# Optimization experiments

Measured on AMD Instinct MI355X. Metric: run time of the kernel, lower is better.

The kernel has to match this reference:

```python
import jax, jax.numpy as jnp
import numpy as np

B, H, W, C, N, P = 4, 200, 176, 256, 16384, 65536
EPS = 1e-3  # BatchNorm eps from the torch module


def _bn(x, g, b, axes):
    # training-mode batch norm (batch statistics), matching nn.BatchNorm forward
    m = x.mean(axes, keepdims=True)
    v = x.var(axes, keepdims=True)
    return (x - m) * jax.lax.rsqrt(v + EPS) * g + b


def setup_inputs() -> dict:
    key = jax.random.key(0)
    ks = jax.random.split(key, 16)
    s = 0.05
    d = {}
    d['feats'] = jax.random.normal(ks[0], (B, C, N), jnp.float32)
    d['cb'] = jax.random.randint(ks[1], (P,), 0, B, dtype=jnp.int32)
    d['cy'] = jax.random.randint(ks[2], (P,), 0, H, dtype=jnp.int32)
    d['cx'] = jax.random.randint(ks[3], (P,), 0, W, dtype=jnp.int32)
    # SH head: Linear(256,256,nb)+BN+ReLU, Linear(256,256,nb)+BN+ReLU, Linear(256,9,b)
    d['sh_w1'] = jax.random.normal(ks[4], (C, 256), jnp.float32) * s
    d['sh_g1'] = jnp.ones((256,), jnp.float32); d['sh_b1'] = jnp.zeros((256,), jnp.float32)
    d['sh_w2'] = jax.random.normal(ks[5], (256, 256), jnp.float32) * s
    d['sh_g2'] = jnp.ones((256,), jnp.float32); d['sh_b2'] = jnp.zeros((256,), jnp.float32)
    d['sh_w3'] = jax.random.normal(ks[6], (256, 9), jnp.float32) * s
    d['sh_bias3'] = jnp.zeros((9,), jnp.float32)
    # Gaus head: Linear(256,256,nb)+BN+ReLU, Linear(256,128,nb)+BN+ReLU, Linear(128,1,b)+sigmoid
    d['g_w1'] = jax.random.normal(ks[7], (C, 256), jnp.float32) * s
    d['g_g1'] = jnp.ones((256,), jnp.float32); d['g_b1'] = jnp.zeros((256,), jnp.float32)
    d['g_w2'] = jax.random.normal(ks[8], (256, 128), jnp.float32) * s
    d['g_g2'] = jnp.ones((128,), jnp.float32); d['g_b2'] = jnp.zeros((128,), jnp.float32)
    d['g_w3'] = jax.random.normal(ks[9], (128, 1), jnp.float32) * s
    d['g_bias3'] = jnp.zeros((1,), jnp.float32)
    # conv_out: 3x3 SparseConv2d no-bias + BN + ReLU ; shared_conv: 3x3 SubMConv2d bias + BN + ReLU
    d['cw1'] = jax.random.normal(ks[10], (3, 3, C, C), jnp.float32) * s
    d['c1_g'] = jnp.ones((C,), jnp.float32); d['c1_b'] = jnp.zeros((C,), jnp.float32)
    d['cw2'] = jax.random.normal(ks[11], (3, 3, C, C), jnp.float32) * s
    d['c2_bias'] = jnp.zeros((C,), jnp.float32)
    d['c2_g'] = jnp.ones((C,), jnp.float32); d['c2_b'] = jnp.zeros((C,), jnp.float32)
    return d


def reference(feats, cb, cy, cx, sh_w1, sh_g1, sh_b1, sh_w2, sh_g2, sh_b2, sh_w3, sh_bias3,
              g_w1, g_g1, g_b1, g_w2, g_g2, g_b2, g_w3, g_bias3,
              cw1, c1_g, c1_b, cw2, c2_bias, c2_g, c2_b):
    # [B,C,N] -> [B*N, C] point-wise features
    pw = feats.transpose(0, 2, 1).reshape(-1, C)
    # pool_feature_in_same_voxel: mean of point features sharing a voxel
    vid = cb * (H * W) + cy * W + cx  # [P] linear voxel id over dense BEV grid
    S = B * H * W
    sums = jax.ops.segment_sum(pw, vid, num_segments=S)            # [S, C]
    cnt = jax.ops.segment_sum(jnp.ones((P,), pw.dtype), vid, num_segments=S)
    pooled = sums / jnp.maximum(cnt, 1.0)[:, None]                 # [S, C]
    # SH head
    h = jax.nn.relu(_bn(pooled @ sh_w1, sh_g1, sh_b1, 0))
    h = jax.nn.relu(_bn(h @ sh_w2, sh_g2, sh_b2, 0))
    pred_sh = h @ sh_w3 + sh_bias3                                 # [S, 9]
    # Gaussian head
    g = jax.nn.relu(_bn(pooled @ g_w1, g_g1, g_b1, 0))
    g = jax.nn.relu(_bn(g @ g_w2, g_g2, g_b2, 0))
    pred_gaus = jax.nn.sigmoid(g @ g_w3 + g_bias3)                 # [S, 1]
    # get_sparse_voxel_feature3: SH (DC term) + gaussian modulated voxel features
    sp = pooled * pred_gaus * pred_sh[:, :1]                       # [S, C]
    x = sp.reshape(B, H, W, C)                                      # dense BEV sparse-tensor equivalent
    dn = ('NHWC', 'HWIO', 'NHWC')
    x = jax.lax.conv_general_dilated(x, cw1, (1, 1), 'SAME', dimension_numbers=dn)
    x = jax.nn.relu(_bn(x, c1_g, c1_b, (0, 1, 2)))
    x = jax.lax.conv_general_dilated(x, cw2, (1, 1), 'SAME', dimension_numbers=dn) + c2_bias
    x = jax.nn.relu(_bn(x, c2_g, c2_b, (0, 1, 2)))
    return x
```

## Files before the change

### kernel.cpp

```cpp
#include <hip/hip_runtime.h>
#include <hip/hip_bf16.h>
#include <cstdint>
#include <cstddef>

#define B_DIM 4
#define H_DIM 200
#define W_DIM 176
#define CCH 256
#define NPP 16384
#define NPTS 65536
#define HW 35200
#define S_TOT 140800
#define EPS 1e-3f
#define INV_S (1.0f/140800.0f)

typedef unsigned short ushort_t;
typedef __attribute__((ext_vector_type(8))) short bf16x8;
typedef __attribute__((ext_vector_type(4))) float f32x4;

__device__ __forceinline__ ushort_t f2bf(float f) {
    __hip_bfloat16 h = __float2bfloat16(f);
    return *(ushort_t*)&h;
}
__device__ __forceinline__ float bf2f(ushort_t u) {
    __hip_bfloat16 h = *(__hip_bfloat16*)&u;
    return __bfloat162float(h);
}

__device__ __forceinline__ void async16(const void* g, void* l) {
    __builtin_amdgcn_global_load_lds(
        (const __attribute__((address_space(1))) unsigned int*)g,
        (__attribute__((address_space(3))) unsigned int*)l,
        16, 0, 0);
}

__device__ __forceinline__ int xcd_virt(int fid, int n) {
    int q = n >> 3, r = n & 7;
    int xcd = fid & 7, idx = fid >> 3;
    int base = (xcd < r) ? xcd * (q + 1) : r * (q + 1) + (xcd - r) * q;
    return base + idx;
}

__global__ __launch_bounds__(256) void k_transpose(
    const float* __restrict__ feats, float* __restrict__ FT)
{
    __shared__ float lds[64][65];
    const int b  = blockIdx.z;
    const int c0 = blockIdx.y * 64;
    const int n0 = blockIdx.x * 64;
    const int tid = threadIdx.x;
#pragma unroll
    for (int i = 0; i < 16; ++i) {
        int idx = i * 256 + tid;
        int cr = idx >> 6, nc = idx & 63;
        lds[cr][nc] = feats[((size_t)b * 256 + c0 + cr) * NPP + n0 + nc];
    }
    __syncthreads();
#pragma unroll
    for (int i = 0; i < 16; ++i) {
        int idx = i * 256 + tid;
        int nr = idx >> 6, cc = idx & 63;
        FT[((size_t)b * NPP + n0 + nr) * CCH + c0 + cc] = lds[cc][nr];
    }
}

__global__ __launch_bounds__(256) void k_buildidx(
    const int* __restrict__ cb, const int* __restrict__ cy,
    const int* __restrict__ cx, int* __restrict__ cnt,
    int* __restrict__ pslot, int* __restrict__ vid)
{
    int p = blockIdx.x * 256 + threadIdx.x;
    int v = cb[p] * HW + cy[p] * W_DIM + cx[p];
    vid[p] = v;
    int r = atomicAdd(&cnt[v], 1);
    if (r < 8) pslot[v * 8 + r] = p;
}

__global__ __launch_bounds__(256) void k_poolgather(
    const float* __restrict__ FT, const int* __restrict__ cnt,
    const int* __restrict__ pslot, const int* __restrict__ vid,
    ushort_t* __restrict__ Pb)
{
    const int wave = threadIdx.x >> 6;
    const int lane = threadIdx.x & 63;
    const int v = blockIdx.x * 4 + wave;
    const int c = cnt[v];
    float4 a = make_float4(0.f, 0.f, 0.f, 0.f);
    if (c <= 8) {
        for (int k = 0; k < c; ++k) {
            int p = pslot[v * 8 + k];
            float4 r = ((const float4*)(FT + (size_t)p * CCH))[lane];
            a.x += r.x; a.y += r.y; a.z += r.z; a.w += r.w;
        }
    } else {
        for (int p = 0; p < NPTS; ++p)
            if (vid[p] == v) {
                float4 r = ((const float4*)(FT + (size_t)p * CCH))[lane];
                a.x += r.x; a.y += r.y; a.z += r.z; a.w += r.w;
            }
    }
    float inv = c ? 1.f / (float)c : 0.f;
    ushort4 o;
    o.x = f2bf(a.x * inv); o.y = f2bf(a.y * inv);
    o.z = f2bf(a.z * inv); o.w = f2bf(a.w * inv);
    ((ushort4*)(Pb + (size_t)v * CCH))[lane] = o;
}

__global__ __launch_bounds__(256) void k_gemmma(
    const ushort_t* __restrict__ X, const ushort_t* __restrict__ Wt,
    ushort_t* __restrict__ Yb, int N, int nblocks)
{
    __shared__ ushort_t Asm[128 * 64];
    __shared__ ushort_t Bsm[128 * 64];
    const int tid  = threadIdx.x;
    const int w    = tid >> 6;
    const int lane = tid & 63;
    const int virt = xcd_virt(blockIdx.x, nblocks);
    int pi, bn;
    if (N == 256) { pi = virt >> 1; bn = (virt & 1) * 128; }
    else          { pi = virt;      bn = 0; }
    const int bm = pi * 128;
    const int wr = (w >> 1) * 64;
    const int wc = (w & 1) * 64;

    size_t aoff[4]; size_t boff[4];
#pragma unroll
    for (int j = 0; j < 4; ++j) {
        int row  = 32 * j + 8 * w + (lane >> 3);
        int qlog = (lane & 7) ^ (row & 7);
        aoff[j] = (size_t)(bm + row) * 256 + qlog * 8;
        boff[j] = (size_t)(bn + row) * 256 + qlog * 8;
    }

    f32x4 acc[4][4] = {};
    for (int kc = 0; kc < 256; kc += 64) {
#pragma unroll
        for (int j = 0; j < 4; ++j)
            async16(X + aoff[j] + kc, Asm + (j * 32 + w * 8) * 64);
#pragma unroll
        for (int j = 0; j < 4; ++j)
            async16(Wt + boff[j] + kc, Bsm + (j * 32 + w * 8) * 64);
        __syncthreads();
#pragma unroll
        for (int ks = 0; ks < 2; ++ks) {
            const int q = ks * 4 + (lane >> 4);
            bf16x8 af[4], bfr[4];
#pragma unroll
            for (int i = 0; i < 4; ++i) {
                int ra = wr + i * 16 + (lane & 15);
                af[i] = *(const bf16x8*)&Asm[ra * 64 + ((q ^ (ra & 7)) * 8)];
            }
#pragma unroll
            for (int jn = 0; jn < 4; ++jn) {
                int rn = wc + jn * 16 + (lane & 15);
                bfr[jn] = *(const bf16x8*)&Bsm[rn * 64 + ((q ^ (rn & 7)) * 8)];
            }
#pragma unroll
            for (int i = 0; i < 4; ++i)
#pragma unroll
                for (int jn = 0; jn < 4; ++jn)
                    acc[i][jn] = __builtin_amdgcn_mfma_f32_16x16x32_bf16(
                        af[i], bfr[jn], acc[i][jn], 0, 0, 0);
        }
        __syncthreads();
    }
    const int crow0 = bm + wr + (lane >> 4) * 4;
    const int ccol0 = bn + wc + (lane & 15);
#pragma unroll
    for (int i = 0; i < 4; ++i)
#pragma unroll
        for (int jn = 0; jn < 4; ++jn)
#pragma unroll
            for (int r = 0; r < 4; ++r)
                Yb[(size_t)(crow0 + i * 16 + r) * N + ccol0 + jn * 16] =
                    f2bf(acc[i][jn][r]);
}

__global__ __launch_bounds__(256) void k_convmma(
    const ushort_t* __restrict__ X, const ushort_t* __restrict__ Wt,
    float* __restrict__ Yf, ushort_t* __restrict__ Yb,
    const float* __restrict__ bias, const ushort_t* __restrict__ zp)
{
    __shared__ ushort_t Asm[2][192 * 64];
    __shared__ ushort_t Bsm[2][128 * 64];
    const int tid  = threadIdx.x;
    const int w    = tid >> 6;
    const int lane = tid & 63;
    const int virt = xcd_virt(blockIdx.x, 2200);
    const int pi   = virt >> 1;
    const int bn   = (virt & 1) * 128;
    const int b    = pi / 275;
    const int rem  = pi % 275;
    const int th   = rem / 11, tw = rem % 11;
    const int y0   = th * 8 - 1, x0 = tw * 16 - 1;
    const int hb   = (w >> 1) * 4;
    const int wc   = (w & 1) * 64;

    const int qlog = (lane & 7) ^ (lane >> 3);
    const ushort_t* asrc[6];
#pragma unroll
    for (int j = 0; j < 6; ++j) {
        int hr = j * 32 + w * 8 + (lane >> 3);
        int ph = hr / 18, pw = hr % 18;
        int y = y0 + ph, x = x0 + pw;
        bool ok = (hr < 180) && ((unsigned)y < (unsigned)H_DIM) &&
                  ((unsigned)x < (unsigned)W_DIM);
        asrc[j] = ok ? X + ((size_t)b * HW + (size_t)y * W_DIM + x) * 256 + qlog * 8
                     : zp + (lane & 7) * 8;
    }
    const ushort_t* bsrc = Wt + (size_t)(bn + w * 8 + (lane >> 3)) * 256 + qlog * 8;
    const int ldsoff = (w * 8) * 64;

#pragma unroll
    for (int j = 0; j < 6; ++j)
        async16(asrc[j], &Asm[0][(j * 32) * 64 + ldsoff]);
#pragma unroll
    for (int j = 0; j < 4; ++j)
        async16(bsrc + (size_t)j * 8192, &Bsm[0][(j * 32) * 64 + ldsoff]);
    __syncthreads();

    f32x4 acc[4][4] = {};
    for (int kc = 0; kc < 4; ++kc) {
        const ushort_t* acur = Asm[kc & 1];
#pragma unroll
        for (int pos = 0; pos < 9; ++pos) {
            const ushort_t* bcur = Bsm[(kc + pos) & 1];
            ushort_t* bnxt = (ushort_t*)Bsm[(kc + pos + 1) & 1];
            if (pos < 8) {
#pragma unroll
                for (int j = 0; j < 4; ++j)
                    async16(bsrc + (size_t)(pos + 1) * 65536 + kc * 64 + j * 8192,
                            bnxt + (j * 32) * 64 + ldsoff);
            } else if (kc < 3) {
#pragma unroll
                for (int j = 0; j < 4; ++j)
                    async16(bsrc + (size_t)(kc + 1) * 64 + j * 8192,
                            bnxt + (j * 32) * 64 + ldsoff);
#pragma unroll
                for (int j = 0; j < 6; ++j)
                    async16(asrc[j] + (kc + 1) * 64,
                            &Asm[(kc + 1) & 1][(j * 32) * 64 + ldsoff]);
            }
            const int dy = pos / 3 - 1, dx = pos % 3 - 1;
#pragma unroll
            for (int ks = 0; ks < 2; ++ks) {
                const int q = ks * 4 + (lane >> 4);
                bf16x8 af[4], bfr[4];
#pragma unroll
                for (int i = 0; i < 4; ++i) {
                    int ri = (hb + i + 1 + dy) * 18 + 1 + dx + (lane & 15);
                    af[i] = *(const bf16x8*)&acur[ri * 64 + ((q ^ (ri & 7)) * 8)];
                }
#pragma unroll
                for (int jn = 0; jn < 4; ++jn) {
                    int rn = wc + jn * 16 + (lane & 15);
                    bfr[jn] = *(const bf16x8*)&bcur[rn * 64 + ((q ^ (rn & 7)) * 8)];
                }
#pragma unroll
                for (int i = 0; i < 4; ++i)
#pragma unroll
                    for (int jn = 0; jn < 4; ++jn)
                        acc[i][jn] = __builtin_amdgcn_mfma_f32_16x16x32_bf16(
                            af[i], bfr[jn], acc[i][jn], 0, 0, 0);
            }
            __syncthreads();
        }
    }

    const size_t sbase = (size_t)b * HW + (size_t)(th * 8) * W_DIM + tw * 16;
    const int colb = bn + wc + (lane & 15);
    const int wsub = (lane >> 4) * 4;
#pragma unroll
    for (int i = 0; i < 4; ++i) {
        int h = hb + i;
#pragma unroll
        for (int jn = 0; jn < 4; ++jn) {
            int col = colb + jn * 16;
            float bb = bias ? bias[col] : 0.f;
#pragma unroll
            for (int r = 0; r < 4; ++r) {
                size_t s = sbase + (size_t)h * W_DIM + wsub + r;
                float v = acc[i][jn][r] + bb;
                size_t o = s * 256 + col;
                if (Yb) Yb[o] = f2bf(v); else Yf[o] = v;
            }
        }
    }
}

__global__ __launch_bounds__(256) void k_castw(
    const float* __restrict__ Wc, ushort_t* __restrict__ Wt, int CO)
{
    int pc = blockIdx.x;
    int co = pc % CO, pos = pc / CO, ci = threadIdx.x;
    Wt[(size_t)pc * 256 + ci] = f2bf(Wc[((size_t)pos * 256 + ci) * CO + co]);
}

__global__ void k_colstats_bf(const ushort_t* __restrict__ Y,
                              float* __restrict__ acc)
{
    const int ncols = blockDim.x;
    const int col = threadIdx.x;
    const int r0 = blockIdx.x * 256;
    float s = 0.f, q = 0.f;
    const ushort_t* p = Y + (size_t)r0 * ncols + col;
    for (int r = 0; r < 256; ++r, p += ncols) {
        float v = bf2f(*p);
        s += v; q += v * v;
    }
    atomicAdd(&acc[col], s);
    atomicAdd(&acc[ncols + col], q);
}

__global__ void k_colstats(const float* __restrict__ Y, float* __restrict__ acc)
{
    const int ncols = blockDim.x;
    const int col = threadIdx.x;
    const int r0 = blockIdx.x * 256;
    float s = 0.f, q = 0.f;
    const float* p = Y + (size_t)r0 * ncols + col;
    for (int r = 0; r < 256; ++r, p += ncols) {
        float v = *p;
        s += v; q += v * v;
    }
    atomicAdd(&acc[col], s);
    atomicAdd(&acc[ncols + col], q);
}

__global__ void k_bnparams(const float* __restrict__ acc,
                           const float* __restrict__ g,
                           const float* __restrict__ b,
                           float* __restrict__ par, int ncols)
{
    int c = threadIdx.x;
    if (c >= ncols) return;
    float m = acc[c] * INV_S;
    float v = acc[ncols + c] * INV_S - m * m;
    float sc = g[c] * rsqrtf(v + EPS);
    par[c] = sc;
    par[ncols + c] = b[c] - m * sc;
}

__global__ __launch_bounds__(256) void k_bnrelu_bf(
    ushort_t* __restrict__ Y, const float* __restrict__ par)
{
    size_t q = (size_t)blockIdx.x * 256 + threadIdx.x;
    int c = (int)(q & 63) * 4;
    ushort4 u = ((ushort4*)Y)[q];
    u.x = f2bf(fmaxf(0.f, bf2f(u.x) * par[c + 0] + par[256 + c + 0]));
    u.y = f2bf(fmaxf(0.f, bf2f(u.y) * par[c + 1] + par[256 + c + 1]));
    u.z = f2bf(fmaxf(0.f, bf2f(u.z) * par[c + 2] + par[256 + c + 2]));
    u.w = f2bf(fmaxf(0.f, bf2f(u.w) * par[c + 3] + par[256 + c + 3]));
    ((ushort4*)Y)[q] = u;
}

__global__ __launch_bounds__(256) void k_headfin(
    const ushort_t* __restrict__ B2, const ushort_t* __restrict__ B3,
    const float* __restrict__ par1, const float* __restrict__ par3,
    const float* __restrict__ shw3, const float* __restrict__ shb3,
    const float* __restrict__ gw3, const float* __restrict__ gb3,
    const ushort_t* __restrict__ Pb, ushort_t* __restrict__ Xb)
{
    const int wave = threadIdx.x >> 6;
    const int lane = threadIdx.x & 63;
    const int s = blockIdx.x * 4 + wave;
    const ushort_t* b2 = B2 + (size_t)s * 256;
    const ushort_t* b3 = B3 + (size_t)s * 128;
    float d1 = 0.f, d2 = 0.f;
    {
        ushort4 u = ((const ushort4*)b2)[lane];
        int c = lane * 4;
        float v0 = fmaxf(0.f, bf2f(u.x) * par1[c + 0] + par1[256 + c + 0]);
        float v1 = fmaxf(0.f, bf2f(u.y) * par1[c + 1] + par1[256 + c + 1]);
        float v2 = fmaxf(0.f, bf2f(u.z) * par1[c + 2] + par1[256 + c + 2]);
        float v3 = fmaxf(0.f, bf2f(u.w) * par1[c + 3] + par1[256 + c + 3]);
        d1 = v0 * shw3[(c + 0) * 9] + v1 * shw3[(c + 1) * 9]
           + v2 * shw3[(c + 2) * 9] + v3 * shw3[(c + 3) * 9];
    }
    {
        ushort2 u = ((const ushort2*)b3)[lane];
        int c = lane * 2;
        float v0 = fmaxf(0.f, bf2f(u.x) * par3[c + 0] + par3[128 + c + 0]);
        float v1 = fmaxf(0.f, bf2f(u.y) * par3[c + 1] + par3[128 + c + 1]);
        d2 = v0 * gw3[c + 0] + v1 * gw3[c + 1];
    }
#pragma unroll
    for (int off = 32; off > 0; off >>= 1) {
        d1 += __shfl_down(d1, off, 64);
        d2 += __shfl_down(d2, off, 64);
    }
    d1 = __shfl(d1, 0, 64);
    d2 = __shfl(d2, 0, 64);
    float shdc = d1 + shb3[0];
    float gaus = 1.f / (1.f + expf(-(d2 + gb3[0])));
    float factor = shdc * gaus;
    ushort4 pv = ((const ushort4*)(Pb + (size_t)s * 256))[lane];
    ushort4 o;
    o.x = f2bf(bf2f(pv.x) * factor);
    o.y = f2bf(bf2f(pv.y) * factor);
    o.z = f2bf(bf2f(pv.z) * factor);
    o.w = f2bf(bf2f(pv.w) * factor);
    ((ushort4*)(Xb + (size_t)s * 256))[lane] = o;
}

__global__ __launch_bounds__(256) void k_bnrelu_inplace(
    float* __restrict__ Y, const float* __restrict__ par)
{
    size_t q = (size_t)blockIdx.x * 256 + threadIdx.x;
    int c = (int)(q & 63) * 4;
    float4* p = (float4*)Y;
    float4 v = p[q];
    v.x = fmaxf(0.f, v.x * par[c + 0] + par[256 + c + 0]);
    v.y = fmaxf(0.f, v.y * par[c + 1] + par[256 + c + 1]);
    v.z = fmaxf(0.f, v.z * par[c + 2] + par[256 + c + 2]);
    v.w = fmaxf(0.f, v.w * par[c + 3] + par[256 + c + 3]);
    p[q] = v;
}

extern "C" void kernel_launch(void* const* d_in, const int* in_sizes, int n_in,
                              void* d_out, int out_size, void* d_ws, size_t ws_size,
                              hipStream_t stream)
{
    (void)in_sizes; (void)n_in; (void)out_size; (void)ws_size;
    const float* feats   = (const float*)d_in[0];
    const int*   cb      = (const int*)d_in[1];
    const int*   cy      = (const int*)d_in[2];
    const int*   cx      = (const int*)d_in[3];
    const float* sh_w1   = (const float*)d_in[4];
    const float* sh_g1   = (const float*)d_in[5];
    const float* sh_b1   = (const float*)d_in[6];
    const float* sh_w2   = (const float*)d_in[7];
    const float* sh_g2   = (const float*)d_in[8];
    const float* sh_b2   = (const float*)d_in[9];
    const float* sh_w3   = (const float*)d_in[10];
    const float* sh_bias3= (const float*)d_in[11];
    const float* g_w1    = (const float*)d_in[12];
    const float* g_g1    = (const float*)d_in[13];
    const float* g_b1    = (const float*)d_in[14];
    const float* g_w2    = (const float*)d_in[15];
    const float* g_g2    = (const float*)d_in[16];
    const float* g_b2    = (const float*)d_in[17];
    const float* g_w3    = (const float*)d_in[18];
    const float* g_bias3 = (const float*)d_in[19];
    const float* cw1     = (const float*)d_in[20];
    const float* c1_g    = (const float*)d_in[21];
    const float* c1_b    = (const float*)d_in[22];
    const float* cw2     = (const float*)d_in[23];
    const float* c2_bias = (const float*)d_in[24];
    const float* c2_g    = (const float*)d_in[25];
    const float* c2_b    = (const float*)d_in[26];

    float* out = (float*)d_out;
    float* ws  = (float*)d_ws;
    ushort_t* Pb   = (ushort_t*)(ws);
    ushort_t* Bb   = (ushort_t*)(ws + 18022400);
    ushort_t* Cb   = (ushort_t*)(ws + 36044800);
    float*    FT   = (float*)(ws + 36044800);
    ushort_t* Db   = (ushort_t*)(ws + 54067200);
    int*      CNTi = (int*)(ws + 54067200);
    int*      PSL  = CNTi + S_TOT;
    int*      VID  = PSL + S_TOT * 8;
    ushort_t* Eb   = (ushort_t*)(ws + 63078400);
    ushort_t* WT1  = (ushort_t*)(ws + 81100800);
    ushort_t* WT2  = WT1 + 589824;
    ushort_t* WS1  = WT2 + 589824;
    ushort_t* WS2  = WS1 + 65536;
    ushort_t* WG1  = WS2 + 65536;
    ushort_t* WG2  = WG1 + 65536;
    ushort_t* ZP   = WG2 + 32768;
    float*    ACC  = (float*)(ZP + 2048);
    float*    PAR  = ACC + 6 * 512;

    hipMemsetAsync(CNTi, 0, (size_t)S_TOT * 4, stream);
    hipMemsetAsync(ACC, 0, 6 * 512 * 4, stream);
    hipMemsetAsync(ZP, 0, 4096, stream);

    k_castw<<<9 * 256, 256, 0, stream>>>(cw1, WT1, 256);
    k_castw<<<9 * 256, 256, 0, stream>>>(cw2, WT2, 256);
    k_castw<<<256, 256, 0, stream>>>(sh_w1, WS1, 256);
    k_castw<<<256, 256, 0, stream>>>(sh_w2, WS2, 256);
    k_castw<<<256, 256, 0, stream>>>(g_w1, WG1, 256);
    k_castw<<<128, 256, 0, stream>>>(g_w2, WG2, 128);

    k_transpose<<<dim3(256, 4, 4), 256, 0, stream>>>(feats, FT);
    k_buildidx<<<NPTS / 256, 256, 0, stream>>>(cb, cy, cx, CNTi, PSL, VID);
    k_poolgather<<<S_TOT / 4, 256, 0, stream>>>(FT, CNTi, PSL, VID, Pb);

    k_gemmma<<<2200, 256, 0, stream>>>(Pb, WS1, Bb, 256, 2200);
    k_colstats_bf<<<550, 256, 0, stream>>>(Bb, ACC + 0 * 512);
    k_bnparams<<<1, 256, 0, stream>>>(ACC + 0 * 512, sh_g1, sh_b1, PAR + 0 * 512, 256);
    k_bnrelu_bf<<<35200, 256, 0, stream>>>(Bb, PAR + 0 * 512);
    k_gemmma<<<2200, 256, 0, stream>>>(Bb, WS2, Cb, 256, 2200);
    k_colstats_bf<<<550, 256, 0, stream>>>(Cb, ACC + 1 * 512);
    k_bnparams<<<1, 256, 0, stream>>>(ACC + 1 * 512, sh_g2, sh_b2, PAR + 1 * 512, 256);
    k_gemmma<<<2200, 256, 0, stream>>>(Pb, WG1, Bb, 256, 2200);
    k_colstats_bf<<<550, 256, 0, stream>>>(Bb, ACC + 2 * 512);
    k_bnparams<<<1, 256, 0, stream>>>(ACC + 2 * 512, g_g1, g_b1, PAR + 2 * 512, 256);
    k_bnrelu_bf<<<35200, 256, 0, stream>>>(Bb, PAR + 2 * 512);
    k_gemmma<<<1100, 256, 0, stream>>>(Bb, WG2, Db, 128, 1100);
    k_colstats_bf<<<550, 128, 0, stream>>>(Db, ACC + 3 * 512);
    k_bnparams<<<1, 128, 0, stream>>>(ACC + 3 * 512, g_g2, g_b2, PAR + 3 * 512, 128);
    k_headfin<<<S_TOT / 4, 256, 0, stream>>>(Cb, Db, PAR + 1 * 512, PAR + 3 * 512,
                                             sh_w3, sh_bias3, g_w3, g_bias3, Pb, Bb);
    k_convmma<<<2200, 256, 0, stream>>>(Bb, WT1, nullptr, Eb, nullptr, ZP);
    k_colstats_bf<<<550, 256, 0, stream>>>(Eb, ACC + 4 * 512);
    k_bnparams<<<1, 256, 0, stream>>>(ACC + 4 * 512, c1_g, c1_b, PAR + 4 * 512, 256);
    k_bnrelu_bf<<<35200, 256, 0, stream>>>(Eb, PAR + 4 * 512);
    k_convmma<<<2200, 256, 0, stream>>>(Eb, WT2, out, nullptr, c2_bias, ZP);
    k_colstats<<<550, 256, 0, stream>>>(out, ACC + 5 * 512);
    k_bnparams<<<1, 256, 0, stream>>>(ACC + 5 * 512, c2_g, c2_b, PAR + 5 * 512, 256);
    k_bnrelu_inplace<<<35200, 256, 0, stream>>>(out, PAR + 5 * 512);
}
```

Baseline: 879.4 us.

## Fuse BN column statistics into GEMM/conv epilogues and merge first-layer head GEMMs

Column sum and sum-of-squares for batch norm are now reduced in the epilogues of the MFMA GEMM and conv kernels (shuffle plus LDS reduction, then atomics), which removes six separate colstats passes that re-read the activations. The SH and Gaussian first-layer weights are concatenated so a single GEMM with N=512 reads the pooled input once and writes two outputs. The statistics are taken from fp32 accumulators rather than bf16-rounded values, which slightly changes the numerics. The epilogues gain extra atomics and a block sync, and the workspace layout is reshuffled, with Eb now aliasing Pb.

New measurement: 865.3 us. No clear change (-1.6%).

```diff
diff --git a/kernel.cpp b/kernel.cpp
--- a/kernel.cpp
+++ b/kernel.cpp
@@ -108,7 +108,9 @@
 
 __global__ __launch_bounds__(256) void k_gemmma(
     const ushort_t* __restrict__ X, const ushort_t* __restrict__ Wt,
-    ushort_t* __restrict__ Yb, int N, int nblocks)
+    ushort_t* __restrict__ Y1, ushort_t* __restrict__ Y2, int ldY,
+    int bnh, int nblocks,
+    float* __restrict__ acc0, float* __restrict__ acc1, int sqoff)
 {
     __shared__ ushort_t Asm[128 * 64];
     __shared__ ushort_t Bsm[128 * 64];
@@ -116,12 +118,11 @@
     const int w    = tid >> 6;
     const int lane = tid & 63;
     const int virt = xcd_virt(blockIdx.x, nblocks);
-    int pi, bn;
-    if (N == 256) { pi = virt >> 1; bn = (virt & 1) * 128; }
-    else          { pi = virt;      bn = 0; }
-    const int bm = pi * 128;
-    const int wr = (w >> 1) * 64;
-    const int wc = (w & 1) * 64;
+    const int pi   = virt / bnh;
+    const int bn   = (virt % bnh) * 128;
+    const int bm   = pi * 128;
+    const int wr   = (w >> 1) * 64;
+    const int wc   = (w & 1) * 64;
 
     size_t aoff[4]; size_t boff[4];
 #pragma unroll
@@ -164,22 +165,56 @@
         }
         __syncthreads();
     }
+
     const int crow0 = bm + wr + (lane >> 4) * 4;
     const int ccol0 = bn + wc + (lane & 15);
+    float ls[4] = {}, lq[4] = {};
 #pragma unroll
     for (int i = 0; i < 4; ++i)
 #pragma unroll
-        for (int jn = 0; jn < 4; ++jn)
-#pragma unroll
-            for (int r = 0; r < 4; ++r)
-                Yb[(size_t)(crow0 + i * 16 + r) * N + ccol0 + jn * 16] =
-                    f2bf(acc[i][jn][r]);
+        for (int jn = 0; jn < 4; ++jn) {
+            int col = ccol0 + jn * 16;
+#pragma unroll
+            for (int r = 0; r < 4; ++r) {
+                float v = acc[i][jn][r];
+                ls[jn] += v; lq[jn] += v * v;
+                size_t row = (size_t)(crow0 + i * 16 + r);
+                if (col < 256) Y1[row * ldY + col] = f2bf(v);
+                else           Y2[row * ldY + col - 256] = f2bf(v);
+            }
+        }
+#pragma unroll
+    for (int jn = 0; jn < 4; ++jn) {
+        ls[jn] += __shfl_xor(ls[jn], 16, 64); ls[jn] += __shfl_xor(ls[jn], 32, 64);
+        lq[jn] += __shfl_xor(lq[jn], 16, 64); lq[jn] += __shfl_xor(lq[jn], 32, 64);
+    }
+    float* red = (float*)Asm;
+    if (lane < 16) {
+#pragma unroll
+        for (int jn = 0; jn < 4; ++jn) {
+            red[((w * 16 + lane) * 4 + jn) * 2 + 0] = ls[jn];
+            red[((w * 16 + lane) * 4 + jn) * 2 + 1] = lq[jn];
+        }
+    }
+    __syncthreads();
+    if (tid < 256) {
+        int colhalf = tid & 127, isq = tid >> 7;
+        int pair = colhalf >> 6, within = colhalf & 63;
+        int l16 = within & 15, jn = within >> 4;
+        int w0 = pair ? 1 : 0, w1 = pair ? 3 : 2;
+        float s = red[((w0 * 16 + l16) * 4 + jn) * 2 + isq]
+                + red[((w1 * 16 + l16) * 4 + jn) * 2 + isq];
+        int colg = bn + colhalf;
+        float* t = (colg < 256) ? acc0 : acc1;
+        atomicAdd(&t[(colg & 255) + isq * sqoff], s);
+    }
 }
 
 __global__ __launch_bounds__(256) void k_convmma(
     const ushort_t* __restrict__ X, const ushort_t* __restrict__ Wt,
     float* __restrict__ Yf, ushort_t* __restrict__ Yb,
-    const float* __restrict__ bias, const ushort_t* __restrict__ zp)
+    const float* __restrict__ bias, const ushort_t* __restrict__ zp,
+    float* __restrict__ accp)
 {
     __shared__ ushort_t Asm[2][192 * 64];
     __shared__ ushort_t Bsm[2][128 * 64];
@@ -270,6 +305,7 @@
     const size_t sbase = (size_t)b * HW + (size_t)(th * 8) * W_DIM + tw * 16;
     const int colb = bn + wc + (lane & 15);
     const int wsub = (lane >> 4) * 4;
+    float ls[4] = {}, lq[4] = {};
 #pragma unroll
     for (int i = 0; i < 4; ++i) {
         int h = hb + i;
@@ -281,10 +317,34 @@
             for (int r = 0; r < 4; ++r) {
                 size_t s = sbase + (size_t)h * W_DIM + wsub + r;
                 float v = acc[i][jn][r] + bb;
+                ls[jn] += v; lq[jn] += v * v;
                 size_t o = s * 256 + col;
                 if (Yb) Yb[o] = f2bf(v); else Yf[o] = v;
             }
         }
+    }
+#pragma unroll
+    for (int jn = 0; jn < 4; ++jn) {
+        ls[jn] += __shfl_xor(ls[jn], 16, 64); ls[jn] += __shfl_xor(ls[jn], 32, 64);
+        lq[jn] += __shfl_xor(lq[jn], 16, 64); lq[jn] += __shfl_xor(lq[jn], 32, 64);
+    }
+    float* red = (float*)&Asm[0][0];
+    if (lane < 16) {
+#pragma unroll
+        for (int jn = 0; jn < 4; ++jn) {
+            red[((w * 16 + lane) * 4 + jn) * 2 + 0] = ls[jn];
+            red[((w * 16 + lane) * 4 + jn) * 2 + 1] = lq[jn];
+        }
+    }
+    __syncthreads();
+    if (tid < 256) {
+        int colhalf = tid & 127, isq = tid >> 7;
+        int pair = colhalf >> 6, within = colhalf & 63;
+        int l16 = within & 15, jn = within >> 4;
+        int w0 = pair ? 1 : 0, w1 = pair ? 3 : 2;
+        float s = red[((w0 * 16 + l16) * 4 + jn) * 2 + isq]
+                + red[((w1 * 16 + l16) * 4 + jn) * 2 + isq];
+        atomicAdd(&accp[(bn + colhalf) + isq * 256], s);
     }
 }
 
@@ -294,37 +354,6 @@
     int pc = blockIdx.x;
     int co = pc % CO, pos = pc / CO, ci = threadIdx.x;
     Wt[(size_t)pc * 256 + ci] = f2bf(Wc[((size_t)pos * 256 + ci) * CO + co]);
-}
-
-__global__ void k_colstats_bf(const ushort_t* __restrict__ Y,
-                              float* __restrict__ acc)
-{
-    const int ncols = blockDim.x;
-    const int col = threadIdx.x;
-    const int r0 = blockIdx.x * 256;
-    float s = 0.f, q = 0.f;
-    const ushort_t* p = Y + (size_t)r0 * ncols + col;
-    for (int r = 0; r < 256; ++r, p += ncols) {
-        float v = bf2f(*p);
-        s += v; q += v * v;
-    }
-    atomicAdd(&acc[col], s);
-    atomicAdd(&acc[ncols + col], q);
-}
-
-__global__ void k_colstats(const float* __restrict__ Y, float* __restrict__ acc)
-{
-    const int ncols = blockDim.x;
-    const int col = threadIdx.x;
-    const int r0 = blockIdx.x * 256;
-    float s = 0.f, q = 0.f;
-    const float* p = Y + (size_t)r0 * ncols + col;
-    for (int r = 0; r < 256; ++r, p += ncols) {
-        float v = *p;
-        s += v; q += v * v;
-    }
-    atomicAdd(&acc[col], s);
-    atomicAdd(&acc[ncols + col], q);
 }
 
 __global__ void k_bnparams(const float* __restrict__ acc,
@@ -453,21 +482,21 @@
     float* out = (float*)d_out;
     float* ws  = (float*)d_ws;
     ushort_t* Pb   = (ushort_t*)(ws);
-    ushort_t* Bb   = (ushort_t*)(ws + 18022400);
-    ushort_t* Cb   = (ushort_t*)(ws + 36044800);
-    float*    FT   = (float*)(ws + 36044800);
-    ushort_t* Db   = (ushort_t*)(ws + 54067200);
-    int*      CNTi = (int*)(ws + 54067200);
+    ushort_t* Bsh  = (ushort_t*)(ws + 18022400);
+    ushort_t* Bg   = (ushort_t*)(ws + 36044800);
+    ushort_t* Cb   = (ushort_t*)(ws + 54067200);
+    float*    FT   = (float*)(ws + 54067200);
+    ushort_t* Db   = (ushort_t*)(ws + 72089600);
+    int*      CNTi = (int*)(ws + 72089600);
     int*      PSL  = CNTi + S_TOT;
     int*      VID  = PSL + S_TOT * 8;
-    ushort_t* Eb   = (ushort_t*)(ws + 63078400);
-    ushort_t* WT1  = (ushort_t*)(ws + 81100800);
+    ushort_t* Eb   = Pb;
+    ushort_t* WCAT = (ushort_t*)(ws + 81100800);
+    ushort_t* WS2  = WCAT + 131072;
+    ushort_t* WG2  = WS2 + 65536;
+    ushort_t* WT1  = WG2 + 32768;
     ushort_t* WT2  = WT1 + 589824;
-    ushort_t* WS1  = WT2 + 589824;
-    ushort_t* WS2  = WS1 + 65536;
-    ushort_t* WG1  = WS2 + 65536;
-    ushort_t* WG2  = WG1 + 65536;
-    ushort_t* ZP   = WG2 + 32768;
+    ushort_t* ZP   = WT2 + 589824;
     float*    ACC  = (float*)(ZP + 2048);
     float*    PAR  = ACC + 6 * 512;
 
@@ -475,39 +504,37 @@
     hipMemsetAsync(ACC, 0, 6 * 512 * 4, stream);
     hipMemsetAsync(ZP, 0, 4096, stream);
 
+    k_castw<<<256, 256, 0, stream>>>(sh_w1, WCAT, 256);
+    k_castw<<<256, 256, 0, stream>>>(g_w1, WCAT + 65536, 256);
+    k_castw<<<256, 256, 0, stream>>>(sh_w2, WS2, 256);
+    k_castw<<<128, 256, 0, stream>>>(g_w2, WG2, 128);
     k_castw<<<9 * 256, 256, 0, stream>>>(cw1, WT1, 256);
     k_castw<<<9 * 256, 256, 0, stream>>>(cw2, WT2, 256);
-    k_castw<<<256, 256, 0, stream>>>(sh_w1, WS1, 256);
-    k_castw<<<256, 256, 0, stream>>>(sh_w2, WS2, 256);
-    k_castw<<<256, 256, 0, stream>>>(g_w1, WG1, 256);
-    k_castw<<<128, 256, 0, stream>>>(g_w2, WG2, 128);
 
     k_transpose<<<dim3(256, 4, 4), 256, 0, stream>>>(feats, FT);
     k_buildidx<<<NPTS / 256, 256, 0, stream>>>(cb, cy, cx, CNTi, PSL, VID);
     k_poolgather<<<S_TOT / 4, 256, 0, stream>>>(FT, CNTi, PSL, VID, Pb);
 
-    k_gemmma<<<2200, 256, 0, stream>>>(Pb, WS1, Bb, 256, 2200);
-    k_colstats_bf<<<550, 256, 0, stream>>>(Bb, ACC + 0 * 512);
+    k_gemmma<<<4400, 256, 0, stream>>>(Pb, WCAT, Bsh, Bg, 256, 4, 4400,
+                                       ACC + 0 * 512, ACC + 2 * 512, 256);
     k_bnparams<<<1, 256, 0, stream>>>(ACC + 0 * 512, sh_g1, sh_b1, PAR + 0 * 512, 256);
-    k_bnrelu_bf<<<35200, 256, 0, stream>>>(Bb, PAR + 0 * 512);
-    k_gemmma<<<2200, 256, 0, stream>>>(Bb, WS2, Cb, 256, 2200);
-    k_colstats_bf<<<550, 256, 0, stream>>>(Cb, ACC + 1 * 512);
+    k_bnparams<<<1, 256, 0, stream>>>(ACC + 2 * 512, g_g1, g_b1, PAR + 2 * 512, 256);
+    k_bnrelu_bf<<<35200, 256, 0, stream>>>(Bsh, PAR + 0 * 512);
+    k_bnrelu_bf<<<35200, 256, 0, stream>>>(Bg, PAR + 2 * 512);
+    k_gemmma<<<2200, 256, 0, stream>>>(Bsh, WS2, Cb, Cb, 256, 2, 2200,
+                                       ACC + 1 * 512, ACC + 1 * 512, 256);
     k_bnparams<<<1, 256, 0, stream>>>(ACC + 1 * 512, sh_g2, sh_b2, PAR + 1 * 512, 256);
-    k_gemmma<<<2200, 256, 0, stream>>>(Pb, WG1, Bb, 256, 2200);
-    k_colstats_bf<<<550, 256, 0, stream>>>(Bb, ACC + 2 * 512);
-    k_bnparams<<<1, 256, 0, stream>>>(ACC + 2 * 512, g_g1, g_b1, PAR + 2 * 512, 256);
-    k_bnrelu_bf<<<35200, 256, 0, stream>>>(Bb, PAR + 2 * 512);
-    k_gemmma<<<1100, 256, 0, stream>>>(Bb, WG2, Db, 128, 1100);
-    k_colstats_bf<<<550, 128, 0, stream>>>(Db, ACC + 3 * 512);
+    k_gemmma<<<1100, 256, 0, stream>>>(Bg, WG2, Db, Db, 128, 1, 1100,
+                                       ACC + 3 * 512, ACC + 3 * 512, 128);
     k_bnparams<<<1, 128, 0, stream>>>(ACC + 3 * 512, g_g2, g_b2, PAR + 3 * 512, 128);
     k_headfin<<<S_TOT / 4, 256, 0, stream>>>(Cb, Db, PAR + 1 * 512, PAR + 3 * 512,
-                                             sh_w3, sh_bias3, g_w3, g_bias3, Pb, Bb);
-    k_convmma<<<2200, 256, 0, stream>>>(Bb, WT1, nullptr, Eb, nullptr, ZP);
-    k_colstats_bf<<<550, 256, 0, stream>>>(Eb, ACC + 4 * 512);
+                                             sh_w3, sh_bias3, g_w3, g_bias3, Pb, Bsh);
+    k_convmma<<<2200, 256, 0, stream>>>(Bsh, WT1, nullptr, Eb, nullptr, ZP,
+                                        ACC + 4 * 512);
     k_bnparams<<<1, 256, 0, stream>>>(ACC + 4 * 512, c1_g, c1_b, PAR + 4 * 512, 256);
     k_bnrelu_bf<<<35200, 256, 0, stream>>>(Eb, PAR + 4 * 512);
-    k_convmma<<<2200, 256, 0, stream>>>(Eb, WT2, out, nullptr, c2_bias, ZP);
-    k_colstats<<<550, 256, 0, stream>>>(out, ACC + 5 * 512);
+    k_convmma<<<2200, 256, 0, stream>>>(Eb, WT2, out, nullptr, c2_bias, ZP,
+                                        ACC + 5 * 512);
     k_bnparams<<<1, 256, 0, stream>>>(ACC + 5 * 512, c2_g, c2_b, PAR + 5 * 512, 256);
     k_bnrelu_inplace<<<35200, 256, 0, stream>>>(out, PAR + 5 * 512);
 }
```
